# Performance work log

Hardware: AMD Instinct MI355X
Metric: run time of the kernel (lower is better)

The kernel has to match this reference:

```python
import jax, jax.numpy as jnp
import numpy as np

MAX_DIST = 8
GUIDANCE_WEIGHT = 0.4
EPS_MAG = 1e-6
EPS_COS = 1e-8
EPS_WSUM = 1e-8


def setup_inputs() -> dict:
    key = jax.random.key(0)
    k1, k2 = jax.random.split(key)
    embeddings = jax.random.normal(k1, (4, 2048, 1024), dtype=jnp.float32)
    guidance_trajectories = jax.random.normal(k2, (512, 1024), dtype=jnp.float32)
    return {"embeddings": embeddings, "guidance_trajectories": guidance_trajectories}


def reference(embeddings, guidance_trajectories):
    B, S, D = embeddings.shape
    W = min(MAX_DIST, S - 1)  # fixed max window size

    # consecutive-token trajectory vectors: diffs[t] = emb[t+1] - emb[t]
    diffs = embeddings[:, 1:, :] - embeddings[:, :-1, :]          # [B, S-1, D]

    # sliding windows of the last W diffs ending at pos-1
    pos = jnp.arange(S)[:, None]                                  # [S, 1]
    k = jnp.arange(W)[None, :]                                    # [1, W]
    idx = pos - W + k                                             # diff index per slot
    valid = (idx >= 0) & (pos >= 1)                               # [S, W]
    windows = diffs[:, jnp.clip(idx, 0, S - 2), :]                # [B, S, W, D]

    # torch.linspace(0.1, 1.0, w) weights, per-position window size w = min(pos, W);
    # valid entries occupy the last w slots of the W-wide window.
    w = jnp.minimum(pos, W)                                       # [S, 1]
    j = k - (W - w)                                               # local index within window
    lin = jnp.where(w > 1, 0.1 + 0.9 * j / jnp.maximum(w - 1, 1), 0.1)
    pos_weights = jnp.where(valid, lin, 0.0).astype(embeddings.dtype)  # [S, W]

    # normalize trajectory vectors, zero where magnitude <= 1e-6
    mag = jnp.linalg.norm(windows, axis=-1, keepdims=True)        # [B, S, W, 1]
    is_valid_mag = mag > EPS_MAG
    normed = jnp.where(is_valid_mag, windows / jnp.where(is_valid_mag, mag, 1.0), 0.0)

    mag_weights = jnp.tanh(mag * 2.0)                             # [B, S, W, 1]
    combined = pos_weights[None, :, :, None] * mag_weights        # [B, S, W, 1]

    # guidance influence: softmax over cosine similarity to guidance bank
    g_norm = jnp.linalg.norm(guidance_trajectories, axis=-1)      # [G]
    a_norm = jnp.linalg.norm(normed, axis=-1)                     # [B, S, W]
    dots = jnp.einsum('bswd,gd->bswg', normed, guidance_trajectories)
    sims = dots / (jnp.maximum(a_norm, EPS_COS)[..., None] * jnp.maximum(g_norm, EPS_COS))
    g_weights = jax.nn.softmax(sims * 2.0, axis=-1)               # [B, S, W, G]
    influence = jnp.einsum('bswg,gd->bswd', g_weights, guidance_trajectories)
    blended = (1.0 - GUIDANCE_WEIGHT) * normed + GUIDANCE_WEIGHT * influence

    weight_sum = jnp.maximum(combined.sum(axis=2), EPS_WSUM)      # [B, S, 1]
    trajectories = (blended * combined).sum(axis=2) / weight_sum  # [B, S, D]
    return trajectories
```

## Files before the change

### kernel.cpp

```cpp
#include <hip/hip_runtime.h>
#include <math.h>

#define B_ 4
#define S_ 2048
#define D_ 1024
#define G_ 512
#define T_ 2047
#define R_ 8188
#define RPAD 8192
#define MT 32
#define ABST 520

typedef __attribute__((ext_vector_type(8))) short short8;
typedef __attribute__((ext_vector_type(4))) short s16x4;
typedef __attribute__((ext_vector_type(4))) float f32x4;

#define WSOFF_RG2  0u
#define WSOFF_MAGW 2048u
#define WSOFF_BP1  34816u
#define WSOFF_BP2  1083392u
#define WSOFF_NH   2131968u
#define WSOFF_IH   18909184u

__device__ inline short to_bf16(float f) {
    union { float f; unsigned u; } v; v.f = f;
    unsigned r = v.u + 0x7fffu + ((v.u >> 16) & 1u);
    return (short)(r >> 16);
}
__device__ inline float fb(unsigned short h) {
    union { unsigned u; float f; } v;
    v.u = ((unsigned)h) << 16;
    return v.f;
}

__global__ __launch_bounds__(64) void prep1_kernel(const float* __restrict__ guid,
                                                   float* __restrict__ rg2,
                                                   short8* __restrict__ Bp1) {
    int g = blockIdx.x, lane = threadIdx.x;
    const float4* gp = (const float4*)(guid + (size_t)g * D_);
    float ss = 0.f;
#pragma unroll
    for (int i = 0; i < 4; ++i) {
        float4 v = gp[lane + 64 * i];
        ss += v.x * v.x + v.y * v.y + v.z * v.z + v.w * v.w;
    }
#pragma unroll
    for (int m = 32; m >= 1; m >>= 1) ss += __shfl_xor(ss, m, 64);
    if (lane == 0) rg2[g] = 2.0f / fmaxf(sqrtf(ss), 1e-8f);
#pragma unroll
    for (int h = 0; h < 2; ++h) {
        int kg = lane + 64 * h;
        const float* src = guid + (size_t)g * D_ + kg * 8;
        short8 v;
#pragma unroll
        for (int j = 0; j < 8; ++j) v[j] = to_bf16(src[j]);
        Bp1[(size_t)kg * G_ + g] = v;
    }
}

__global__ __launch_bounds__(256) void prep2_kernel(const float* __restrict__ guid,
                                                    short8* __restrict__ Bp2) {
    int gg = blockIdx.x, tid = threadIdx.x;
#pragma unroll
    for (int dd = 0; dd < 4; ++dd) {
        int d = tid + 256 * dd;
        short8 v;
#pragma unroll
        for (int j = 0; j < 8; ++j) v[j] = to_bf16(guid[(size_t)(gg * 8 + j) * D_ + d]);
        Bp2[(size_t)gg * D_ + d] = v;
    }
}

__global__ __launch_bounds__(1024, 4) void fused_kernel(const float* __restrict__ emb,
                                                        const short8* __restrict__ Bp1,
                                                        const short8* __restrict__ Bp2,
                                                        const float* __restrict__ rg2,
                                                        float* __restrict__ magw,
                                                        short* __restrict__ normh,
                                                        short* __restrict__ inflh) {
    __shared__ short AB[MT][ABST];
    __shared__ float rg2s[G_];
    __shared__ float pred[MT][16];
    __shared__ float redmx[MT], redrs[MT];

    const int tid = threadIdx.x;
    const int wave = tid >> 6, lane = tid & 63;
    const int l15 = lane & 15, quad = lane >> 4;
    const int r0 = blockIdx.x * MT;

    if (tid < G_) rg2s[tid] = rg2[tid];

    s16x4 hold[2][2];
#pragma unroll
    for (int i = 0; i < 2; ++i) {
        int rr = wave * 2 + i;
        int R = r0 + rr;
        if (R < R_) {
            int b = R / T_;
            int t = R - b * T_;
            const float4* p = (const float4*)(emb + ((size_t)b * S_ + t) * D_);
            float4 dv[4]; float ss = 0.f;
#pragma unroll
            for (int j = 0; j < 4; ++j) {
                float4 x0 = p[lane + 64 * j];
                float4 x1 = p[lane + 64 * j + 256];
                dv[j] = make_float4(x1.x - x0.x, x1.y - x0.y, x1.z - x0.z, x1.w - x0.w);
                ss += dv[j].x * dv[j].x + dv[j].y * dv[j].y + dv[j].z * dv[j].z + dv[j].w * dv[j].w;
            }
#pragma unroll
            for (int m = 32; m >= 1; m >>= 1) ss += __shfl_xor(ss, m, 64);
            float mag = sqrtf(ss);
            float rmag = (mag > 1e-6f) ? (1.0f / mag) : 0.0f;
            if (lane == 0) magw[R] = tanhf(2.0f * mag);
            s16x4 h[4];
#pragma unroll
            for (int j = 0; j < 4; ++j) {
                h[j][0] = to_bf16(dv[j].x * rmag); h[j][1] = to_bf16(dv[j].y * rmag);
                h[j][2] = to_bf16(dv[j].z * rmag); h[j][3] = to_bf16(dv[j].w * rmag);
            }
            short* nb = normh + (size_t)R * D_ + 4 * lane;
#pragma unroll
            for (int j = 0; j < 4; ++j) *(s16x4*)(nb + 256 * j) = h[j];
            *(s16x4*)&AB[rr][4 * lane] = h[0];
            *(s16x4*)&AB[rr][4 * lane + 256] = h[1];
            hold[i][0] = h[2]; hold[i][1] = h[3];
        } else {
            s16x4 z = (s16x4)0;
            *(s16x4*)&AB[rr][4 * lane] = z;
            *(s16x4*)&AB[rr][4 * lane + 256] = z;
            hold[i][0] = z; hold[i][1] = z;
        }
    }
    __syncthreads();

    f32x4 acc1[2][2];
#pragma unroll
    for (int mt = 0; mt < 2; ++mt)
#pragma unroll
        for (int nt = 0; nt < 2; ++nt) acc1[mt][nt] = (f32x4)0.f;
#pragma unroll
    for (int p = 0; p < 2; ++p) {
        if (p == 1) {
            __syncthreads();
#pragma unroll
            for (int i = 0; i < 2; ++i) {
                int rr = wave * 2 + i;
                *(s16x4*)&AB[rr][4 * lane] = hold[i][0];
                *(s16x4*)&AB[rr][4 * lane + 256] = hold[i][1];
            }
            __syncthreads();
        }
        const short8* Bb = Bp1 + ((size_t)(64 * p + quad)) * G_ + wave * 32 + l15;
        short8 bc0 = Bb[0], bc1 = Bb[16], bn0, bn1;
        for (int ks = 0; ks < 16; ++ks) {
            if (ks < 15) {
                const short8* Bx = Bb + (size_t)(ks + 1) * 4 * G_;
                bn0 = Bx[0]; bn1 = Bx[16];
            }
            short8 a0 = *(const short8*)&AB[l15][ks * 32 + quad * 8];
            short8 a1 = *(const short8*)&AB[16 + l15][ks * 32 + quad * 8];
            acc1[0][0] = __builtin_amdgcn_mfma_f32_16x16x32_bf16(a0, bc0, acc1[0][0], 0, 0, 0);
            acc1[0][1] = __builtin_amdgcn_mfma_f32_16x16x32_bf16(a0, bc1, acc1[0][1], 0, 0, 0);
            acc1[1][0] = __builtin_amdgcn_mfma_f32_16x16x32_bf16(a1, bc0, acc1[1][0], 0, 0, 0);
            acc1[1][1] = __builtin_amdgcn_mfma_f32_16x16x32_bf16(a1, bc1, acc1[1][1], 0, 0, 0);
            bc0 = bn0; bc1 = bn1;
        }
    }

    {
        float pmax[2][4];
#pragma unroll
        for (int mt = 0; mt < 2; ++mt)
#pragma unroll
            for (int r2 = 0; r2 < 4; ++r2) pmax[mt][r2] = -1e30f;
#pragma unroll
        for (int mt = 0; mt < 2; ++mt)
#pragma unroll
            for (int nt = 0; nt < 2; ++nt) {
                float rgv = rg2s[wave * 32 + nt * 16 + l15];
#pragma unroll
                for (int r2 = 0; r2 < 4; ++r2) {
                    float lg = acc1[mt][nt][r2] * rgv;
                    acc1[mt][nt][r2] = lg;
                    pmax[mt][r2] = fmaxf(pmax[mt][r2], lg);
                }
            }
#pragma unroll
        for (int m = 8; m >= 1; m >>= 1)
#pragma unroll
            for (int mt = 0; mt < 2; ++mt)
#pragma unroll
                for (int r2 = 0; r2 < 4; ++r2)
                    pmax[mt][r2] = fmaxf(pmax[mt][r2], __shfl_xor(pmax[mt][r2], m, 16));
        if (l15 == 0) {
#pragma unroll
            for (int mt = 0; mt < 2; ++mt)
#pragma unroll
                for (int r2 = 0; r2 < 4; ++r2)
                    pred[mt * 16 + quad * 4 + r2][wave] = pmax[mt][r2];
        }
        __syncthreads();
        if (tid < MT) {
            float m = pred[tid][0];
#pragma unroll
            for (int w2 = 1; w2 < 16; ++w2) m = fmaxf(m, pred[tid][w2]);
            redmx[tid] = m;
        }
        __syncthreads();
        float psum[2][4];
#pragma unroll
        for (int mt = 0; mt < 2; ++mt)
#pragma unroll
            for (int r2 = 0; r2 < 4; ++r2) psum[mt][r2] = 0.f;
#pragma unroll
        for (int mt = 0; mt < 2; ++mt)
#pragma unroll
            for (int nt = 0; nt < 2; ++nt)
#pragma unroll
                for (int r2 = 0; r2 < 4; ++r2) {
                    float e = __expf(acc1[mt][nt][r2] - redmx[mt * 16 + quad * 4 + r2]);
                    acc1[mt][nt][r2] = e;
                    psum[mt][r2] += e;
                }
#pragma unroll
        for (int m = 8; m >= 1; m >>= 1)
#pragma unroll
            for (int mt = 0; mt < 2; ++mt)
#pragma unroll
                for (int r2 = 0; r2 < 4; ++r2)
                    psum[mt][r2] += __shfl_xor(psum[mt][r2], m, 16);
        if (l15 == 0) {
#pragma unroll
            for (int mt = 0; mt < 2; ++mt)
#pragma unroll
                for (int r2 = 0; r2 < 4; ++r2)
                    pred[mt * 16 + quad * 4 + r2][wave] = psum[mt][r2];
        }
        __syncthreads();
        if (tid < MT) {
            float s = 0.f;
#pragma unroll
            for (int w2 = 0; w2 < 16; ++w2) s += pred[tid][w2];
            redrs[tid] = 1.0f / s;
        }
        __syncthreads();
#pragma unroll
        for (int mt = 0; mt < 2; ++mt)
#pragma unroll
            for (int nt = 0; nt < 2; ++nt)
#pragma unroll
                for (int r2 = 0; r2 < 4; ++r2) {
                    int row = mt * 16 + quad * 4 + r2;
                    AB[row][wave * 32 + nt * 16 + l15] =
                        to_bf16(acc1[mt][nt][r2] * redrs[row]);
                }
    }
    __syncthreads();

    f32x4 acc2[2][4];
#pragma unroll
    for (int mt = 0; mt < 2; ++mt)
#pragma unroll
        for (int nt = 0; nt < 4; ++nt) acc2[mt][nt] = (f32x4)0.f;
    {
        const short8* Bb = Bp2 + (size_t)quad * D_ + wave * 64 + l15;
        short8 bc[4], bn[4];
#pragma unroll
        for (int nt = 0; nt < 4; ++nt) bc[nt] = Bb[nt * 16];
        for (int ks = 0; ks < 16; ++ks) {
            if (ks < 15) {
                const short8* Bx = Bb + (size_t)(ks + 1) * 4 * D_;
#pragma unroll
                for (int nt = 0; nt < 4; ++nt) bn[nt] = Bx[nt * 16];
            }
            short8 a0 = *(const short8*)&AB[l15][ks * 32 + quad * 8];
            short8 a1 = *(const short8*)&AB[16 + l15][ks * 32 + quad * 8];
#pragma unroll
            for (int nt = 0; nt < 4; ++nt) {
                acc2[0][nt] = __builtin_amdgcn_mfma_f32_16x16x32_bf16(a0, bc[nt], acc2[0][nt], 0, 0, 0);
                acc2[1][nt] = __builtin_amdgcn_mfma_f32_16x16x32_bf16(a1, bc[nt], acc2[1][nt], 0, 0, 0);
            }
#pragma unroll
            for (int nt = 0; nt < 4; ++nt) bc[nt] = bn[nt];
        }
    }

#pragma unroll
    for (int mt = 0; mt < 2; ++mt)
#pragma unroll
        for (int nt = 0; nt < 4; ++nt) {
            int d = wave * 64 + nt * 16 + l15;
#pragma unroll
            for (int r2 = 0; r2 < 4; ++r2) {
                int R = r0 + mt * 16 + quad * 4 + r2;
                if (R < R_) inflh[(size_t)R * D_ + d] = to_bf16(acc2[mt][nt][r2]);
            }
        }
}

__global__ __launch_bounds__(256) void combine_kernel(const float* __restrict__ magw,
                                                      const unsigned short* __restrict__ normh,
                                                      const unsigned short* __restrict__ inflh,
                                                      float* __restrict__ out) {
    int blk = blockIdx.x;
    int b = blk >> 8;
    int rem = blk & 255;
    int s0 = (rem >> 1) * 16;
    int d = (rem & 1) * 512 + threadIdx.x * 2;
    size_t rbase = (size_t)b * T_;

    float2 ring[8]; float mring[8];
#pragma unroll
    for (int a2 = 0; a2 < 8; ++a2) { ring[a2] = make_float2(0.f, 0.f); mring[a2] = 0.f; }

#define LOADBL(t_, dst_)                                                        \
    {                                                                           \
        size_t off_ = (rbase + (t_)) * D_ + d;                                  \
        ushort2 n2_ = *(const ushort2*)(normh + off_);                          \
        ushort2 i2_ = *(const ushort2*)(inflh + off_);                          \
        dst_ = make_float2(0.6f * fb(n2_.x) + 0.4f * fb(i2_.x),                 \
                           0.6f * fb(n2_.y) + 0.4f * fb(i2_.y));                \
    }

#pragma unroll
    for (int a2 = 0; a2 < 7; ++a2) {
        int t = s0 - 8 + a2;
        if (t >= 0) {
            LOADBL(t, ring[a2]);
            mring[a2] = magw[rbase + t];
        }
    }
    if (s0 != 0) {
#pragma unroll
        for (int i = 0; i < 16; ++i) {
            int t = s0 + i - 1;
            LOADBL(t, ring[(i + 7) & 7]);
            mring[(i + 7) & 7] = magw[rbase + t];
            float2 acc = make_float2(0.f, 0.f); float wsum = 0.f;
#pragma unroll
            for (int a = 1; a <= 8; ++a) {
                int slot = (i - a) & 7;
                float lin = 0.1f + (0.9f / 7.0f) * (float)(8 - a);
                float wt = lin * mring[slot];
                acc.x += wt * ring[slot].x; acc.y += wt * ring[slot].y;
                wsum += wt;
            }
            float rws = 1.0f / fmaxf(wsum, 1e-8f);
            *(float2*)&out[((size_t)b * S_ + s0 + i) * D_ + d] =
                make_float2(acc.x * rws, acc.y * rws);
        }
    } else {
#pragma unroll
        for (int i = 0; i < 16; ++i) {
            if (i >= 1) {
                int t = i - 1;
                LOADBL(t, ring[(i + 7) & 7]);
                mring[(i + 7) & 7] = magw[rbase + t];
            }
            int w = (i < 8) ? i : 8;
            float rw = (w > 1) ? 0.9f / (float)(w - 1) : 0.0f;
            float2 acc = make_float2(0.f, 0.f); float wsum = 0.f;
            for (int a = 1; a <= w; ++a) {
                int slot = (i - a) & 7;
                float lin = 0.1f + rw * (float)(w - a);
                float wt = lin * mring[slot];
                acc.x += wt * ring[slot].x; acc.y += wt * ring[slot].y;
                wsum += wt;
            }
            float rws = 1.0f / fmaxf(wsum, 1e-8f);
            *(float2*)&out[((size_t)b * S_ + i) * D_ + d] =
                make_float2(acc.x * rws, acc.y * rws);
        }
    }
#undef LOADBL
}

extern "C" void kernel_launch(void* const* d_in, const int* in_sizes, int n_in,
                              void* d_out, int out_size, void* d_ws, size_t ws_size,
                              hipStream_t stream) {
    const float* emb  = (const float*)d_in[0];
    const float* guid = (const float*)d_in[1];
    float* out = (float*)d_out;
    char* ws = (char*)d_ws;

    float*  rg2   = (float*)(ws + WSOFF_RG2);
    float*  magw  = (float*)(ws + WSOFF_MAGW);
    short8* Bp1   = (short8*)(ws + WSOFF_BP1);
    short8* Bp2   = (short8*)(ws + WSOFF_BP2);
    short*  normh = (short*)(ws + WSOFF_NH);
    short*  inflh = (short*)(ws + WSOFF_IH);

    prep1_kernel<<<G_, 64, 0, stream>>>(guid, rg2, Bp1);
    prep2_kernel<<<G_ / 8, 256, 0, stream>>>(guid, Bp2);
    fused_kernel<<<RPAD / MT, 1024, 0, stream>>>(emb, Bp1, Bp2, rg2, magw, normh, inflh);
    combine_kernel<<<B_ * 128 * 2, 256, 0, stream>>>(magw, (const unsigned short*)normh,
                                                     (const unsigned short*)inflh, out);
}
```

Measured before the change: 129.1 us.

## Halve fused kernel row tile to 16 and merge guidance prep kernels

The fused GEMM-softmax-GEMM kernel now processes 16 rows per block instead of 32. The whole 1024-wide normalized row fits in LDS at once, which removes the two-pass K staging and its extra barriers. The launch bound now asks for higher occupancy, and the two guidance preprocessing kernels are merged into one launch. The cost is that each block's guidance B-matrix loads are reused across half as many rows, so global/L2 traffic for Bp1/Bp2 doubles.

New measurement: 139.1 us. +7.7%, slower.

```diff
diff --git a/kernel.cpp b/kernel.cpp
--- a/kernel.cpp
+++ b/kernel.cpp
@@ -8,8 +8,8 @@
 #define T_ 2047
 #define R_ 8188
 #define RPAD 8192
-#define MT 32
-#define ABST 520
+#define MT 16
+#define ABST 1032
 
 typedef __attribute__((ext_vector_type(8))) short short8;
 typedef __attribute__((ext_vector_type(4))) short s16x4;
@@ -33,45 +33,47 @@
     return v.f;
 }
 
-__global__ __launch_bounds__(64) void prep1_kernel(const float* __restrict__ guid,
+__global__ __launch_bounds__(256) void prep_kernel(const float* __restrict__ guid,
                                                    float* __restrict__ rg2,
-                                                   short8* __restrict__ Bp1) {
-    int g = blockIdx.x, lane = threadIdx.x;
-    const float4* gp = (const float4*)(guid + (size_t)g * D_);
-    float ss = 0.f;
-#pragma unroll
-    for (int i = 0; i < 4; ++i) {
-        float4 v = gp[lane + 64 * i];
-        ss += v.x * v.x + v.y * v.y + v.z * v.z + v.w * v.w;
-    }
-#pragma unroll
-    for (int m = 32; m >= 1; m >>= 1) ss += __shfl_xor(ss, m, 64);
-    if (lane == 0) rg2[g] = 2.0f / fmaxf(sqrtf(ss), 1e-8f);
-#pragma unroll
-    for (int h = 0; h < 2; ++h) {
-        int kg = lane + 64 * h;
-        const float* src = guid + (size_t)g * D_ + kg * 8;
-        short8 v;
-#pragma unroll
-        for (int j = 0; j < 8; ++j) v[j] = to_bf16(src[j]);
-        Bp1[(size_t)kg * G_ + g] = v;
-    }
-}
-
-__global__ __launch_bounds__(256) void prep2_kernel(const float* __restrict__ guid,
-                                                    short8* __restrict__ Bp2) {
-    int gg = blockIdx.x, tid = threadIdx.x;
-#pragma unroll
-    for (int dd = 0; dd < 4; ++dd) {
-        int d = tid + 256 * dd;
-        short8 v;
-#pragma unroll
-        for (int j = 0; j < 8; ++j) v[j] = to_bf16(guid[(size_t)(gg * 8 + j) * D_ + d]);
-        Bp2[(size_t)gg * D_ + d] = v;
-    }
-}
-
-__global__ __launch_bounds__(1024, 4) void fused_kernel(const float* __restrict__ emb,
+                                                   short8* __restrict__ Bp1,
+                                                   short8* __restrict__ Bp2) {
+    int bid = blockIdx.x, tid = threadIdx.x;
+    if (bid < 128) {
+        int wave = tid >> 6, lane = tid & 63;
+        int g = bid * 4 + wave;
+        const float4* gp = (const float4*)(guid + (size_t)g * D_);
+        float ss = 0.f;
+#pragma unroll
+        for (int i = 0; i < 4; ++i) {
+            float4 v = gp[lane + 64 * i];
+            ss += v.x * v.x + v.y * v.y + v.z * v.z + v.w * v.w;
+        }
+#pragma unroll
+        for (int m = 32; m >= 1; m >>= 1) ss += __shfl_xor(ss, m, 64);
+        if (lane == 0) rg2[g] = 2.0f / fmaxf(sqrtf(ss), 1e-8f);
+#pragma unroll
+        for (int h = 0; h < 2; ++h) {
+            int kg = lane + 64 * h;
+            const float* src = guid + (size_t)g * D_ + kg * 8;
+            short8 v;
+#pragma unroll
+            for (int j = 0; j < 8; ++j) v[j] = to_bf16(src[j]);
+            Bp1[(size_t)kg * G_ + g] = v;
+        }
+    } else {
+        int gg = bid - 128;
+#pragma unroll
+        for (int dd = 0; dd < 4; ++dd) {
+            int d = tid + 256 * dd;
+            short8 v;
+#pragma unroll
+            for (int j = 0; j < 8; ++j) v[j] = to_bf16(guid[(size_t)(gg * 8 + j) * D_ + d]);
+            Bp2[(size_t)gg * D_ + d] = v;
+        }
+    }
+}
+
+__global__ __launch_bounds__(1024, 8) void fused_kernel(const float* __restrict__ emb,
                                                         const short8* __restrict__ Bp1,
                                                         const short8* __restrict__ Bp2,
                                                         const float* __restrict__ rg2,
@@ -90,10 +92,8 @@
 
     if (tid < G_) rg2s[tid] = rg2[tid];
 
-    s16x4 hold[2][2];
-#pragma unroll
-    for (int i = 0; i < 2; ++i) {
-        int rr = wave * 2 + i;
+    {
+        int rr = wave;
         int R = r0 + rr;
         if (R < R_) {
             int b = R / T_;
@@ -112,188 +112,140 @@
             float mag = sqrtf(ss);
             float rmag = (mag > 1e-6f) ? (1.0f / mag) : 0.0f;
             if (lane == 0) magw[R] = tanhf(2.0f * mag);
-            s16x4 h[4];
+            short* nb = normh + (size_t)R * D_ + 4 * lane;
 #pragma unroll
             for (int j = 0; j < 4; ++j) {
-                h[j][0] = to_bf16(dv[j].x * rmag); h[j][1] = to_bf16(dv[j].y * rmag);
-                h[j][2] = to_bf16(dv[j].z * rmag); h[j][3] = to_bf16(dv[j].w * rmag);
-            }
-            short* nb = normh + (size_t)R * D_ + 4 * lane;
-#pragma unroll
-            for (int j = 0; j < 4; ++j) *(s16x4*)(nb + 256 * j) = h[j];
-            *(s16x4*)&AB[rr][4 * lane] = h[0];
-            *(s16x4*)&AB[rr][4 * lane + 256] = h[1];
-            hold[i][0] = h[2]; hold[i][1] = h[3];
+                s16x4 h;
+                h[0] = to_bf16(dv[j].x * rmag); h[1] = to_bf16(dv[j].y * rmag);
+                h[2] = to_bf16(dv[j].z * rmag); h[3] = to_bf16(dv[j].w * rmag);
+                *(s16x4*)(nb + 256 * j) = h;
+                *(s16x4*)&AB[rr][4 * lane + 256 * j] = h;
+            }
         } else {
             s16x4 z = (s16x4)0;
-            *(s16x4*)&AB[rr][4 * lane] = z;
-            *(s16x4*)&AB[rr][4 * lane + 256] = z;
-            hold[i][0] = z; hold[i][1] = z;
+#pragma unroll
+            for (int j = 0; j < 4; ++j) *(s16x4*)&AB[rr][4 * lane + 256 * j] = z;
         }
     }
     __syncthreads();
 
-    f32x4 acc1[2][2];
-#pragma unroll
-    for (int mt = 0; mt < 2; ++mt)
-#pragma unroll
-        for (int nt = 0; nt < 2; ++nt) acc1[mt][nt] = (f32x4)0.f;
-#pragma unroll
-    for (int p = 0; p < 2; ++p) {
-        if (p == 1) {
-            __syncthreads();
-#pragma unroll
-            for (int i = 0; i < 2; ++i) {
-                int rr = wave * 2 + i;
-                *(s16x4*)&AB[rr][4 * lane] = hold[i][0];
-                *(s16x4*)&AB[rr][4 * lane + 256] = hold[i][1];
-            }
-            __syncthreads();
-        }
-        const short8* Bb = Bp1 + ((size_t)(64 * p + quad)) * G_ + wave * 32 + l15;
+    f32x4 acc1[2];
+    acc1[0] = (f32x4)0.f; acc1[1] = (f32x4)0.f;
+    {
+        const short8* Bb = Bp1 + (size_t)quad * G_ + wave * 32 + l15;
+        short8 bc0 = Bb[0], bc1 = Bb[16], bn0, bn1;
+        for (int ks = 0; ks < 32; ++ks) {
+            if (ks < 31) {
+                const short8* Bx = Bb + (size_t)(ks + 1) * 4 * G_;
+                bn0 = Bx[0]; bn1 = Bx[16];
+            }
+            short8 a0 = *(const short8*)&AB[l15][ks * 32 + quad * 8];
+            acc1[0] = __builtin_amdgcn_mfma_f32_16x16x32_bf16(a0, bc0, acc1[0], 0, 0, 0);
+            acc1[1] = __builtin_amdgcn_mfma_f32_16x16x32_bf16(a0, bc1, acc1[1], 0, 0, 0);
+            bc0 = bn0; bc1 = bn1;
+        }
+    }
+
+    {
+        float pmax[4];
+#pragma unroll
+        for (int r2 = 0; r2 < 4; ++r2) pmax[r2] = -1e30f;
+#pragma unroll
+        for (int nt = 0; nt < 2; ++nt) {
+            float rgv = rg2s[wave * 32 + nt * 16 + l15];
+#pragma unroll
+            for (int r2 = 0; r2 < 4; ++r2) {
+                float lg = acc1[nt][r2] * rgv;
+                acc1[nt][r2] = lg;
+                pmax[r2] = fmaxf(pmax[r2], lg);
+            }
+        }
+#pragma unroll
+        for (int m = 8; m >= 1; m >>= 1)
+#pragma unroll
+            for (int r2 = 0; r2 < 4; ++r2)
+                pmax[r2] = fmaxf(pmax[r2], __shfl_xor(pmax[r2], m, 16));
+        if (l15 == 0) {
+#pragma unroll
+            for (int r2 = 0; r2 < 4; ++r2)
+                pred[quad * 4 + r2][wave] = pmax[r2];
+        }
+        __syncthreads();
+        if (tid < MT) {
+            float m = pred[tid][0];
+#pragma unroll
+            for (int w2 = 1; w2 < 16; ++w2) m = fmaxf(m, pred[tid][w2]);
+            redmx[tid] = m;
+        }
+        __syncthreads();
+        float psum[4];
+#pragma unroll
+        for (int r2 = 0; r2 < 4; ++r2) psum[r2] = 0.f;
+#pragma unroll
+        for (int nt = 0; nt < 2; ++nt)
+#pragma unroll
+            for (int r2 = 0; r2 < 4; ++r2) {
+                float e = __expf(acc1[nt][r2] - redmx[quad * 4 + r2]);
+                acc1[nt][r2] = e;
+                psum[r2] += e;
+            }
+#pragma unroll
+        for (int m = 8; m >= 1; m >>= 1)
+#pragma unroll
+            for (int r2 = 0; r2 < 4; ++r2)
+                psum[r2] += __shfl_xor(psum[r2], m, 16);
+        if (l15 == 0) {
+#pragma unroll
+            for (int r2 = 0; r2 < 4; ++r2)
+                pred[quad * 4 + r2][wave] = psum[r2];
+        }
+        __syncthreads();
+        if (tid < MT) {
+            float s = 0.f;
+#pragma unroll
+            for (int w2 = 0; w2 < 16; ++w2) s += pred[tid][w2];
+            redrs[tid] = 1.0f / s;
+        }
+        __syncthreads();
+#pragma unroll
+        for (int nt = 0; nt < 2; ++nt)
+#pragma unroll
+            for (int r2 = 0; r2 < 4; ++r2) {
+                int row = quad * 4 + r2;
+                AB[row][wave * 32 + nt * 16 + l15] =
+                    to_bf16(acc1[nt][r2] * redrs[row]);
+            }
+    }
+    __syncthreads();
+
+    f32x4 acc2[4];
+#pragma unroll
+    for (int nt = 0; nt < 4; ++nt) acc2[nt] = (f32x4)0.f;
+#pragma unroll
+    for (int half = 0; half < 2; ++half) {
+        const short8* Bb = Bp2 + (size_t)quad * D_ + wave * 64 + half * 32 + l15;
         short8 bc0 = Bb[0], bc1 = Bb[16], bn0, bn1;
         for (int ks = 0; ks < 16; ++ks) {
             if (ks < 15) {
-                const short8* Bx = Bb + (size_t)(ks + 1) * 4 * G_;
+                const short8* Bx = Bb + (size_t)(ks + 1) * 4 * D_;
                 bn0 = Bx[0]; bn1 = Bx[16];
             }
             short8 a0 = *(const short8*)&AB[l15][ks * 32 + quad * 8];
-            short8 a1 = *(const short8*)&AB[16 + l15][ks * 32 + quad * 8];
-            acc1[0][0] = __builtin_amdgcn_mfma_f32_16x16x32_bf16(a0, bc0, acc1[0][0], 0, 0, 0);
-            acc1[0][1] = __builtin_amdgcn_mfma_f32_16x16x32_bf16(a0, bc1, acc1[0][1], 0, 0, 0);
-            acc1[1][0] = __builtin_amdgcn_mfma_f32_16x16x32_bf16(a1, bc0, acc1[1][0], 0, 0, 0);
-            acc1[1][1] = __builtin_amdgcn_mfma_f32_16x16x32_bf16(a1, bc1, acc1[1][1], 0, 0, 0);
+            acc2[half * 2 + 0] = __builtin_amdgcn_mfma_f32_16x16x32_bf16(a0, bc0, acc2[half * 2 + 0], 0, 0, 0);
+            acc2[half * 2 + 1] = __builtin_amdgcn_mfma_f32_16x16x32_bf16(a0, bc1, acc2[half * 2 + 1], 0, 0, 0);
             bc0 = bn0; bc1 = bn1;
         }
     }
 
-    {
-        float pmax[2][4];
-#pragma unroll
-        for (int mt = 0; mt < 2; ++mt)
-#pragma unroll
-            for (int r2 = 0; r2 < 4; ++r2) pmax[mt][r2] = -1e30f;
-#pragma unroll
-        for (int mt = 0; mt < 2; ++mt)
-#pragma unroll
-            for (int nt = 0; nt < 2; ++nt) {
-                float rgv = rg2s[wave * 32 + nt * 16 + l15];
-#pragma unroll
-                for (int r2 = 0; r2 < 4; ++r2) {
-                    float lg = acc1[mt][nt][r2] * rgv;
-                    acc1[mt][nt][r2] = lg;
-                    pmax[mt][r2] = fmaxf(pmax[mt][r2], lg);
-                }
-            }
-#pragma unroll
-        for (int m = 8; m >= 1; m >>= 1)
-#pragma unroll
-            for (int mt = 0; mt < 2; ++mt)
-#pragma unroll
-                for (int r2 = 0; r2 < 4; ++r2)
-                    pmax[mt][r2] = fmaxf(pmax[mt][r2], __shfl_xor(pmax[mt][r2], m, 16));
-        if (l15 == 0) {
-#pragma unroll
-            for (int mt = 0; mt < 2; ++mt)
-#pragma unroll
-                for (int r2 = 0; r2 < 4; ++r2)
-                    pred[mt * 16 + quad * 4 + r2][wave] = pmax[mt][r2];
-        }
-        __syncthreads();
-        if (tid < MT) {
-            float m = pred[tid][0];
-#pragma unroll
-            for (int w2 = 1; w2 < 16; ++w2) m = fmaxf(m, pred[tid][w2]);
-            redmx[tid] = m;
-        }
-        __syncthreads();
-        float psum[2][4];
-#pragma unroll
-        for (int mt = 0; mt < 2; ++mt)
-#pragma unroll
-            for (int r2 = 0; r2 < 4; ++r2) psum[mt][r2] = 0.f;
-#pragma unroll
-        for (int mt = 0; mt < 2; ++mt)
-#pragma unroll
-            for (int nt = 0; nt < 2; ++nt)
-#pragma unroll
-                for (int r2 = 0; r2 < 4; ++r2) {
-                    float e = __expf(acc1[mt][nt][r2] - redmx[mt * 16 + quad * 4 + r2]);
-                    acc1[mt][nt][r2] = e;
-                    psum[mt][r2] += e;
-                }
-#pragma unroll
-        for (int m = 8; m >= 1; m >>= 1)
-#pragma unroll
-            for (int mt = 0; mt < 2; ++mt)
-#pragma unroll
-                for (int r2 = 0; r2 < 4; ++r2)
-                    psum[mt][r2] += __shfl_xor(psum[mt][r2], m, 16);
-        if (l15 == 0) {
-#pragma unroll
-            for (int mt = 0; mt < 2; ++mt)
-#pragma unroll
-                for (int r2 = 0; r2 < 4; ++r2)
-                    pred[mt * 16 + quad * 4 + r2][wave] = psum[mt][r2];
-        }
-        __syncthreads();
-        if (tid < MT) {
-            float s = 0.f;
-#pragma unroll
-            for (int w2 = 0; w2 < 16; ++w2) s += pred[tid][w2];
-            redrs[tid] = 1.0f / s;
-        }
-        __syncthreads();
-#pragma unroll
-        for (int mt = 0; mt < 2; ++mt)
-#pragma unroll
-            for (int nt = 0; nt < 2; ++nt)
-#pragma unroll
-                for (int r2 = 0; r2 < 4; ++r2) {
-                    int row = mt * 16 + quad * 4 + r2;
-                    AB[row][wave * 32 + nt * 16 + l15] =
-                        to_bf16(acc1[mt][nt][r2] * redrs[row]);
-                }
-    }
-    __syncthreads();
-
-    f32x4 acc2[2][4];
-#pragma unroll
-    for (int mt = 0; mt < 2; ++mt)
-#pragma unroll
-        for (int nt = 0; nt < 4; ++nt) acc2[mt][nt] = (f32x4)0.f;
-    {
-        const short8* Bb = Bp2 + (size_t)quad * D_ + wave * 64 + l15;
-        short8 bc[4], bn[4];
-#pragma unroll
-        for (int nt = 0; nt < 4; ++nt) bc[nt] = Bb[nt * 16];
-        for (int ks = 0; ks < 16; ++ks) {
-            if (ks < 15) {
-                const short8* Bx = Bb + (size_t)(ks + 1) * 4 * D_;
-#pragma unroll
-                for (int nt = 0; nt < 4; ++nt) bn[nt] = Bx[nt * 16];
-            }
-            short8 a0 = *(const short8*)&AB[l15][ks * 32 + quad * 8];
-            short8 a1 = *(const short8*)&AB[16 + l15][ks * 32 + quad * 8];
-#pragma unroll
-            for (int nt = 0; nt < 4; ++nt) {
-                acc2[0][nt] = __builtin_amdgcn_mfma_f32_16x16x32_bf16(a0, bc[nt], acc2[0][nt], 0, 0, 0);
-                acc2[1][nt] = __builtin_amdgcn_mfma_f32_16x16x32_bf16(a1, bc[nt], acc2[1][nt], 0, 0, 0);
-            }
-#pragma unroll
-            for (int nt = 0; nt < 4; ++nt) bc[nt] = bn[nt];
-        }
-    }
-
-#pragma unroll
-    for (int mt = 0; mt < 2; ++mt)
-#pragma unroll
-        for (int nt = 0; nt < 4; ++nt) {
-            int d = wave * 64 + nt * 16 + l15;
+#pragma unroll
+    for (int half = 0; half < 2; ++half)
+#pragma unroll
+        for (int ntl = 0; ntl < 2; ++ntl) {
+            int d = wave * 64 + half * 32 + ntl * 16 + l15;
 #pragma unroll
             for (int r2 = 0; r2 < 4; ++r2) {
-                int R = r0 + mt * 16 + quad * 4 + r2;
-                if (R < R_) inflh[(size_t)R * D_ + d] = to_bf16(acc2[mt][nt][r2]);
+                int R = r0 + quad * 4 + r2;
+                if (R < R_) inflh[(size_t)R * D_ + d] = to_bf16(acc2[half * 2 + ntl][r2]);
             }
         }
 }
@@ -390,8 +342,7 @@
     short*  normh = (short*)(ws + WSOFF_NH);
     short*  inflh = (short*)(ws + WSOFF_IH);
 
-    prep1_kernel<<<G_, 64, 0, stream>>>(guid, rg2, Bp1);
-    prep2_kernel<<<G_ / 8, 256, 0, stream>>>(guid, Bp2);
+    prep_kernel<<<192, 256, 0, stream>>>(guid, rg2, Bp1, Bp2);
     fused_kernel<<<RPAD / MT, 1024, 0, stream>>>(emb, Bp1, Bp2, rg2, magw, normh, inflh);
     combine_kernel<<<B_ * 128 * 2, 256, 0, stream>>>(magw, (const unsigned short*)normh,
                                                      (const unsigned short*)inflh, out);
```

## Defer normalization scaling to overlap diff loads with first GEMM half

Applied to the files above, without the earlier changes.

The fused kernel now writes unnormalized bf16 diffs for the first half of D and starts the first MFMA pass immediately. The second-half embedding loads are held in registers and finished after that pass, so the magnitude reduction no longer blocks the GEMM. The 1/mag scale is applied to the logits and passed to the combine kernel through a new rmag array. Also merges the two prep kernels into one launch and widens combine to 4 elements per thread with prefetching of the next row. This trades extra register pressure for the overlap, and skipping the normalization before bf16 rounding may change precision slightly.

Measured after the change: 127.0 us. No clear change (-1.6%).

```diff
diff --git a/kernel.cpp b/kernel.cpp
--- a/kernel.cpp
+++ b/kernel.cpp
@@ -14,13 +14,15 @@
 typedef __attribute__((ext_vector_type(8))) short short8;
 typedef __attribute__((ext_vector_type(4))) short s16x4;
 typedef __attribute__((ext_vector_type(4))) float f32x4;
+typedef __attribute__((ext_vector_type(4))) unsigned short u16x4;
 
 #define WSOFF_RG2  0u
 #define WSOFF_MAGW 2048u
-#define WSOFF_BP1  34816u
-#define WSOFF_BP2  1083392u
-#define WSOFF_NH   2131968u
-#define WSOFF_IH   18909184u
+#define WSOFF_RMAG 34816u
+#define WSOFF_BP1  67584u
+#define WSOFF_BP2  1116160u
+#define WSOFF_NH   2164736u
+#define WSOFF_IH   18941952u
 
 __device__ inline short to_bf16(float f) {
     union { float f; unsigned u; } v; v.f = f;
@@ -33,41 +35,43 @@
     return v.f;
 }
 
-__global__ __launch_bounds__(64) void prep1_kernel(const float* __restrict__ guid,
+__global__ __launch_bounds__(256) void prep_kernel(const float* __restrict__ guid,
                                                    float* __restrict__ rg2,
-                                                   short8* __restrict__ Bp1) {
-    int g = blockIdx.x, lane = threadIdx.x;
-    const float4* gp = (const float4*)(guid + (size_t)g * D_);
-    float ss = 0.f;
-#pragma unroll
-    for (int i = 0; i < 4; ++i) {
-        float4 v = gp[lane + 64 * i];
-        ss += v.x * v.x + v.y * v.y + v.z * v.z + v.w * v.w;
-    }
-#pragma unroll
-    for (int m = 32; m >= 1; m >>= 1) ss += __shfl_xor(ss, m, 64);
-    if (lane == 0) rg2[g] = 2.0f / fmaxf(sqrtf(ss), 1e-8f);
-#pragma unroll
-    for (int h = 0; h < 2; ++h) {
-        int kg = lane + 64 * h;
-        const float* src = guid + (size_t)g * D_ + kg * 8;
-        short8 v;
-#pragma unroll
-        for (int j = 0; j < 8; ++j) v[j] = to_bf16(src[j]);
-        Bp1[(size_t)kg * G_ + g] = v;
-    }
-}
-
-__global__ __launch_bounds__(256) void prep2_kernel(const float* __restrict__ guid,
-                                                    short8* __restrict__ Bp2) {
-    int gg = blockIdx.x, tid = threadIdx.x;
-#pragma unroll
-    for (int dd = 0; dd < 4; ++dd) {
-        int d = tid + 256 * dd;
-        short8 v;
-#pragma unroll
-        for (int j = 0; j < 8; ++j) v[j] = to_bf16(guid[(size_t)(gg * 8 + j) * D_ + d]);
-        Bp2[(size_t)gg * D_ + d] = v;
+                                                   short8* __restrict__ Bp1,
+                                                   short8* __restrict__ Bp2) {
+    int bid = blockIdx.x, tid = threadIdx.x;
+    if (bid < 128) {
+        int wave = tid >> 6, lane = tid & 63;
+        int g = bid * 4 + wave;
+        const float4* gp = (const float4*)(guid + (size_t)g * D_);
+        float ss = 0.f;
+#pragma unroll
+        for (int i = 0; i < 4; ++i) {
+            float4 v = gp[lane + 64 * i];
+            ss += v.x * v.x + v.y * v.y + v.z * v.z + v.w * v.w;
+        }
+#pragma unroll
+        for (int m = 32; m >= 1; m >>= 1) ss += __shfl_xor(ss, m, 64);
+        if (lane == 0) rg2[g] = 2.0f / fmaxf(sqrtf(ss), 1e-8f);
+#pragma unroll
+        for (int h = 0; h < 2; ++h) {
+            int kg = lane + 64 * h;
+            const float* src = guid + (size_t)g * D_ + kg * 8;
+            short8 v;
+#pragma unroll
+            for (int j = 0; j < 8; ++j) v[j] = to_bf16(src[j]);
+            Bp1[(size_t)kg * G_ + g] = v;
+        }
+    } else {
+        int gg = bid - 128;
+#pragma unroll
+        for (int dd = 0; dd < 4; ++dd) {
+            int d = tid + 256 * dd;
+            short8 v;
+#pragma unroll
+            for (int j = 0; j < 8; ++j) v[j] = to_bf16(guid[(size_t)(gg * 8 + j) * D_ + d]);
+            Bp2[(size_t)gg * D_ + d] = v;
+        }
     }
 }
 
@@ -76,12 +80,14 @@
                                                         const short8* __restrict__ Bp2,
                                                         const float* __restrict__ rg2,
                                                         float* __restrict__ magw,
+                                                        float* __restrict__ rmagA,
                                                         short* __restrict__ normh,
                                                         short* __restrict__ inflh) {
     __shared__ short AB[MT][ABST];
     __shared__ float rg2s[G_];
     __shared__ float pred[MT][16];
     __shared__ float redmx[MT], redrs[MT];
+    __shared__ float rmagS[MT];
 
     const int tid = threadIdx.x;
     const int wave = tid >> 6, lane = tid & 63;
@@ -90,67 +96,61 @@
 
     if (tid < G_) rg2s[tid] = rg2[tid];
 
-    s16x4 hold[2][2];
+    float4 hx0[2][2], hx1[2][2];
+    float ssp[2];
+    int Rrow[2];
 #pragma unroll
     for (int i = 0; i < 2; ++i) {
         int rr = wave * 2 + i;
         int R = r0 + rr;
+        Rrow[i] = R;
         if (R < R_) {
             int b = R / T_;
             int t = R - b * T_;
             const float4* p = (const float4*)(emb + ((size_t)b * S_ + t) * D_);
-            float4 dv[4]; float ss = 0.f;
-#pragma unroll
-            for (int j = 0; j < 4; ++j) {
+            float ss = 0.f;
+            short* nb = normh + (size_t)R * D_ + 4 * lane;
+#pragma unroll
+            for (int j = 0; j < 2; ++j) {
                 float4 x0 = p[lane + 64 * j];
                 float4 x1 = p[lane + 64 * j + 256];
-                dv[j] = make_float4(x1.x - x0.x, x1.y - x0.y, x1.z - x0.z, x1.w - x0.w);
-                ss += dv[j].x * dv[j].x + dv[j].y * dv[j].y + dv[j].z * dv[j].z + dv[j].w * dv[j].w;
-            }
-#pragma unroll
-            for (int m = 32; m >= 1; m >>= 1) ss += __shfl_xor(ss, m, 64);
-            float mag = sqrtf(ss);
-            float rmag = (mag > 1e-6f) ? (1.0f / mag) : 0.0f;
-            if (lane == 0) magw[R] = tanhf(2.0f * mag);
-            s16x4 h[4];
-#pragma unroll
-            for (int j = 0; j < 4; ++j) {
-                h[j][0] = to_bf16(dv[j].x * rmag); h[j][1] = to_bf16(dv[j].y * rmag);
-                h[j][2] = to_bf16(dv[j].z * rmag); h[j][3] = to_bf16(dv[j].w * rmag);
-            }
-            short* nb = normh + (size_t)R * D_ + 4 * lane;
-#pragma unroll
-            for (int j = 0; j < 4; ++j) *(s16x4*)(nb + 256 * j) = h[j];
-            *(s16x4*)&AB[rr][4 * lane] = h[0];
-            *(s16x4*)&AB[rr][4 * lane + 256] = h[1];
-            hold[i][0] = h[2]; hold[i][1] = h[3];
+                float4 dv = make_float4(x1.x - x0.x, x1.y - x0.y, x1.z - x0.z, x1.w - x0.w);
+                ss += dv.x * dv.x + dv.y * dv.y + dv.z * dv.z + dv.w * dv.w;
+                s16x4 h;
+                h[0] = to_bf16(dv.x); h[1] = to_bf16(dv.y);
+                h[2] = to_bf16(dv.z); h[3] = to_bf16(dv.w);
+                *(s16x4*)(nb + 256 * j) = h;
+                *(s16x4*)&AB[rr][4 * lane + 256 * j] = h;
+            }
+            ssp[i] = ss;
+#pragma unroll
+            for (int j = 0; j < 2; ++j) {
+                hx0[i][j] = p[lane + 64 * (j + 2)];
+                hx1[i][j] = p[lane + 64 * (j + 2) + 256];
+            }
         } else {
             s16x4 z = (s16x4)0;
             *(s16x4*)&AB[rr][4 * lane] = z;
             *(s16x4*)&AB[rr][4 * lane + 256] = z;
-            hold[i][0] = z; hold[i][1] = z;
-        }
-    }
-    __syncthreads();
+            ssp[i] = 0.f;
+#pragma unroll
+            for (int j = 0; j < 2; ++j) {
+                hx0[i][j] = make_float4(0.f, 0.f, 0.f, 0.f);
+                hx1[i][j] = make_float4(0.f, 0.f, 0.f, 0.f);
+            }
+        }
+    }
+    __builtin_amdgcn_sched_barrier(0);
+    asm volatile("s_waitcnt lgkmcnt(0)" ::: "memory");
+    __builtin_amdgcn_s_barrier();
 
     f32x4 acc1[2][2];
 #pragma unroll
     for (int mt = 0; mt < 2; ++mt)
 #pragma unroll
         for (int nt = 0; nt < 2; ++nt) acc1[mt][nt] = (f32x4)0.f;
-#pragma unroll
-    for (int p = 0; p < 2; ++p) {
-        if (p == 1) {
-            __syncthreads();
-#pragma unroll
-            for (int i = 0; i < 2; ++i) {
-                int rr = wave * 2 + i;
-                *(s16x4*)&AB[rr][4 * lane] = hold[i][0];
-                *(s16x4*)&AB[rr][4 * lane + 256] = hold[i][1];
-            }
-            __syncthreads();
-        }
-        const short8* Bb = Bp1 + ((size_t)(64 * p + quad)) * G_ + wave * 32 + l15;
+    {
+        const short8* Bb = Bp1 + (size_t)quad * G_ + wave * 32 + l15;
         short8 bc0 = Bb[0], bc1 = Bb[16], bn0, bn1;
         for (int ks = 0; ks < 16; ++ks) {
             if (ks < 15) {
@@ -167,7 +167,70 @@
         }
     }
 
+    s16x4 holdh[2][2];
+#pragma unroll
+    for (int i = 0; i < 2; ++i) {
+        int R = Rrow[i];
+        int rr = wave * 2 + i;
+        float ss = ssp[i];
+        if (R < R_) {
+            short* nb = normh + (size_t)R * D_ + 4 * lane;
+#pragma unroll
+            for (int j = 0; j < 2; ++j) {
+                float4 dv = make_float4(hx1[i][j].x - hx0[i][j].x, hx1[i][j].y - hx0[i][j].y,
+                                        hx1[i][j].z - hx0[i][j].z, hx1[i][j].w - hx0[i][j].w);
+                ss += dv.x * dv.x + dv.y * dv.y + dv.z * dv.z + dv.w * dv.w;
+                s16x4 h;
+                h[0] = to_bf16(dv.x); h[1] = to_bf16(dv.y);
+                h[2] = to_bf16(dv.z); h[3] = to_bf16(dv.w);
+                *(s16x4*)(nb + 256 * (j + 2)) = h;
+                holdh[i][j] = h;
+            }
+        } else {
+            holdh[i][0] = (s16x4)0; holdh[i][1] = (s16x4)0;
+        }
+#pragma unroll
+        for (int m = 32; m >= 1; m >>= 1) ss += __shfl_xor(ss, m, 64);
+        float mag = sqrtf(ss);
+        float rmag = (mag > 1e-6f) ? (1.0f / mag) : 0.0f;
+        if (lane == 0) {
+            rmagS[rr] = rmag;
+            if (R < R_) { magw[R] = tanhf(2.0f * mag); rmagA[R] = rmag; }
+        }
+    }
+    __syncthreads();
+#pragma unroll
+    for (int i = 0; i < 2; ++i) {
+        int rr = wave * 2 + i;
+        *(s16x4*)&AB[rr][4 * lane] = holdh[i][0];
+        *(s16x4*)&AB[rr][4 * lane + 256] = holdh[i][1];
+    }
+    __syncthreads();
+
     {
+        const short8* Bb = Bp1 + (size_t)(64 + quad) * G_ + wave * 32 + l15;
+        short8 bc0 = Bb[0], bc1 = Bb[16], bn0, bn1;
+        for (int ks = 0; ks < 16; ++ks) {
+            if (ks < 15) {
+                const short8* Bx = Bb + (size_t)(ks + 1) * 4 * G_;
+                bn0 = Bx[0]; bn1 = Bx[16];
+            }
+            short8 a0 = *(const short8*)&AB[l15][ks * 32 + quad * 8];
+            short8 a1 = *(const short8*)&AB[16 + l15][ks * 32 + quad * 8];
+            acc1[0][0] = __builtin_amdgcn_mfma_f32_16x16x32_bf16(a0, bc0, acc1[0][0], 0, 0, 0);
+            acc1[0][1] = __builtin_amdgcn_mfma_f32_16x16x32_bf16(a0, bc1, acc1[0][1], 0, 0, 0);
+            acc1[1][0] = __builtin_amdgcn_mfma_f32_16x16x32_bf16(a1, bc0, acc1[1][0], 0, 0, 0);
+            acc1[1][1] = __builtin_amdgcn_mfma_f32_16x16x32_bf16(a1, bc1, acc1[1][1], 0, 0, 0);
+            bc0 = bn0; bc1 = bn1;
+        }
+    }
+
+    {
+        float rmv[2][4];
+#pragma unroll
+        for (int mt = 0; mt < 2; ++mt)
+#pragma unroll
+            for (int r2 = 0; r2 < 4; ++r2) rmv[mt][r2] = rmagS[mt * 16 + quad * 4 + r2];
         float pmax[2][4];
 #pragma unroll
         for (int mt = 0; mt < 2; ++mt)
@@ -180,7 +243,7 @@
                 float rgv = rg2s[wave * 32 + nt * 16 + l15];
 #pragma unroll
                 for (int r2 = 0; r2 < 4; ++r2) {
-                    float lg = acc1[mt][nt][r2] * rgv;
+                    float lg = acc1[mt][nt][r2] * rgv * rmv[mt][r2];
                     acc1[mt][nt][r2] = lg;
                     pmax[mt][r2] = fmaxf(pmax[mt][r2], lg);
                 }
@@ -299,80 +362,108 @@
 }
 
 __global__ __launch_bounds__(256) void combine_kernel(const float* __restrict__ magw,
+                                                      const float* __restrict__ rmagA,
                                                       const unsigned short* __restrict__ normh,
                                                       const unsigned short* __restrict__ inflh,
                                                       float* __restrict__ out) {
     int blk = blockIdx.x;
-    int b = blk >> 8;
-    int rem = blk & 255;
-    int s0 = (rem >> 1) * 16;
-    int d = (rem & 1) * 512 + threadIdx.x * 2;
+    int b = blk >> 7;
+    int s0 = (blk & 127) * 16;
+    int d0 = threadIdx.x * 4;
     size_t rbase = (size_t)b * T_;
 
-    float2 ring[8]; float mring[8];
-#pragma unroll
-    for (int a2 = 0; a2 < 8; ++a2) { ring[a2] = make_float2(0.f, 0.f); mring[a2] = 0.f; }
-
-#define LOADBL(t_, dst_)                                                        \
-    {                                                                           \
-        size_t off_ = (rbase + (t_)) * D_ + d;                                  \
-        ushort2 n2_ = *(const ushort2*)(normh + off_);                          \
-        ushort2 i2_ = *(const ushort2*)(inflh + off_);                          \
-        dst_ = make_float2(0.6f * fb(n2_.x) + 0.4f * fb(i2_.x),                 \
-                           0.6f * fb(n2_.y) + 0.4f * fb(i2_.y));                \
-    }
-
-#pragma unroll
-    for (int a2 = 0; a2 < 7; ++a2) {
-        int t = s0 - 8 + a2;
-        if (t >= 0) {
-            LOADBL(t, ring[a2]);
-            mring[a2] = magw[rbase + t];
-        }
-    }
+    f32x4 ring[8]; float mring[8];
+#pragma unroll
+    for (int j = 0; j < 8; ++j) { ring[j] = (f32x4)0.f; mring[j] = 0.f; }
+
+#define BLEND(n4_, i4_, ns_, dst_)                                       \
+    {                                                                    \
+        dst_[0] = ns_ * fb(n4_[0]) + 0.4f * fb(i4_[0]);                  \
+        dst_[1] = ns_ * fb(n4_[1]) + 0.4f * fb(i4_[1]);                  \
+        dst_[2] = ns_ * fb(n4_[2]) + 0.4f * fb(i4_[2]);                  \
+        dst_[3] = ns_ * fb(n4_[3]) + 0.4f * fb(i4_[3]);                  \
+    }
+
     if (s0 != 0) {
 #pragma unroll
+        for (int j = 0; j < 8; ++j) {
+            int t = s0 - 8 + j;
+            size_t off = (rbase + t) * D_ + d0;
+            u16x4 n4 = *(const u16x4*)(normh + off);
+            u16x4 i4 = *(const u16x4*)(inflh + off);
+            float ns = 0.6f * rmagA[rbase + t];
+            BLEND(n4, i4, ns, ring[j]);
+            mring[j] = magw[rbase + t];
+        }
+#pragma unroll
         for (int i = 0; i < 16; ++i) {
-            int t = s0 + i - 1;
-            LOADBL(t, ring[(i + 7) & 7]);
-            mring[(i + 7) & 7] = magw[rbase + t];
-            float2 acc = make_float2(0.f, 0.f); float wsum = 0.f;
+            u16x4 pn = (u16x4)0, pi = (u16x4)0; float pm = 0.f, pr = 0.f;
+            if (i < 15) {
+                int t = s0 + i;
+                size_t off = (rbase + t) * D_ + d0;
+                pn = *(const u16x4*)(normh + off);
+                pi = *(const u16x4*)(inflh + off);
+                pm = magw[rbase + t];
+                pr = rmagA[rbase + t];
+            }
+            f32x4 acc = (f32x4)0.f; float wsum = 0.f;
 #pragma unroll
             for (int a = 1; a <= 8; ++a) {
                 int slot = (i - a) & 7;
-                float lin = 0.1f + (0.9f / 7.0f) * (float)(8 - a);
+                const float lin = 0.1f + (0.9f / 7.0f) * (float)(8 - a);
                 float wt = lin * mring[slot];
-                acc.x += wt * ring[slot].x; acc.y += wt * ring[slot].y;
+                acc[0] += wt * ring[slot][0]; acc[1] += wt * ring[slot][1];
+                acc[2] += wt * ring[slot][2]; acc[3] += wt * ring[slot][3];
                 wsum += wt;
             }
             float rws = 1.0f / fmaxf(wsum, 1e-8f);
-            *(float2*)&out[((size_t)b * S_ + s0 + i) * D_ + d] =
-                make_float2(acc.x * rws, acc.y * rws);
+            f32x4 o; o[0] = acc[0] * rws; o[1] = acc[1] * rws; o[2] = acc[2] * rws; o[3] = acc[3] * rws;
+            *(f32x4*)&out[((size_t)b * S_ + s0 + i) * D_ + d0] = o;
+            if (i < 15) {
+                float ns = 0.6f * pr;
+                BLEND(pn, pi, ns, ring[i & 7]);
+                mring[i & 7] = pm;
+            }
         }
     } else {
 #pragma unroll
         for (int i = 0; i < 16; ++i) {
-            if (i >= 1) {
-                int t = i - 1;
-                LOADBL(t, ring[(i + 7) & 7]);
-                mring[(i + 7) & 7] = magw[rbase + t];
-            }
-            int w = (i < 8) ? i : 8;
-            float rw = (w > 1) ? 0.9f / (float)(w - 1) : 0.0f;
-            float2 acc = make_float2(0.f, 0.f); float wsum = 0.f;
-            for (int a = 1; a <= w; ++a) {
-                int slot = (i - a) & 7;
-                float lin = 0.1f + rw * (float)(w - a);
-                float wt = lin * mring[slot];
-                acc.x += wt * ring[slot].x; acc.y += wt * ring[slot].y;
-                wsum += wt;
+            u16x4 pn = (u16x4)0, pi = (u16x4)0; float pm = 0.f, pr = 0.f;
+            if (i < 15) {
+                int t = i;
+                size_t off = (rbase + t) * D_ + d0;
+                pn = *(const u16x4*)(normh + off);
+                pi = *(const u16x4*)(inflh + off);
+                pm = magw[rbase + t];
+                pr = rmagA[rbase + t];
+            }
+            const int w = (i < 8) ? i : 8;
+            f32x4 acc = (f32x4)0.f; float wsum = 0.f;
+            if (w > 0) {
+                const float rw = (w > 1) ? 0.9f / (float)(w - 1) : 0.0f;
+#pragma unroll
+                for (int a = 1; a <= 8; ++a) {
+                    if (a <= w) {
+                        int slot = (i - a) & 7;
+                        float lin = 0.1f + rw * (float)(w - a);
+                        float wt = lin * mring[slot];
+                        acc[0] += wt * ring[slot][0]; acc[1] += wt * ring[slot][1];
+                        acc[2] += wt * ring[slot][2]; acc[3] += wt * ring[slot][3];
+                        wsum += wt;
+                    }
+                }
             }
             float rws = 1.0f / fmaxf(wsum, 1e-8f);
-            *(float2*)&out[((size_t)b * S_ + i) * D_ + d] =
-                make_float2(acc.x * rws, acc.y * rws);
-        }
-    }
-#undef LOADBL
+            f32x4 o; o[0] = acc[0] * rws; o[1] = acc[1] * rws; o[2] = acc[2] * rws; o[3] = acc[3] * rws;
+            *(f32x4*)&out[((size_t)b * S_ + i) * D_ + d0] = o;
+            if (i < 15) {
+                float ns = 0.6f * pr;
+                BLEND(pn, pi, ns, ring[i & 7]);
+                mring[i & 7] = pm;
+            }
+        }
+    }
+#undef BLEND
 }
 
 extern "C" void kernel_launch(void* const* d_in, const int* in_sizes, int n_in,
@@ -385,14 +476,14 @@
 
     float*  rg2   = (float*)(ws + WSOFF_RG2);
     float*  magw  = (float*)(ws + WSOFF_MAGW);
+    float*  rmagA = (float*)(ws + WSOFF_RMAG);
     short8* Bp1   = (short8*)(ws + WSOFF_BP1);
     short8* Bp2   = (short8*)(ws + WSOFF_BP2);
     short*  normh = (short*)(ws + WSOFF_NH);
     short*  inflh = (short*)(ws + WSOFF_IH);
 
-    prep1_kernel<<<G_, 64, 0, stream>>>(guid, rg2, Bp1);
-    prep2_kernel<<<G_ / 8, 256, 0, stream>>>(guid, Bp2);
-    fused_kernel<<<RPAD / MT, 1024, 0, stream>>>(emb, Bp1, Bp2, rg2, magw, normh, inflh);
-    combine_kernel<<<B_ * 128 * 2, 256, 0, stream>>>(magw, (const unsigned short*)normh,
-                                                     (const unsigned short*)inflh, out);
-}
+    prep_kernel<<<192, 256, 0, stream>>>(guid, rg2, Bp1, Bp2);
+    fused_kernel<<<RPAD / MT, 1024, 0, stream>>>(emb, Bp1, Bp2, rg2, magw, rmagA, normh, inflh);
+    combine_kernel<<<B_ * 128, 256, 0, stream>>>(magw, rmagA, (const unsigned short*)normh,
+                                                 (const unsigned short*)inflh, out);
+}
```
